# Performance work log

Hardware: AMD Instinct MI355X
Metric: run time of the kernel (lower is better)

Reference implementation:

```python
import jax, jax.numpy as jnp
import numpy as np

N = 262144        # number of nodes
D = 64            # fixed in-degree per destination node (edges grouped by dest)
RATIO = 0.5
K = int(D * RATIO)  # edges kept per node = 32


def setup_inputs() -> dict:
    key = jax.random.key(0)
    k1, k2 = jax.random.split(key)
    logits = jax.random.normal(k1, (N,), dtype=jnp.float32)
    # source endpoints: random nodes; destination endpoints: sorted, D edges per node
    src = jax.random.randint(k2, (N * D,), 0, N, dtype=jnp.int32)
    dst = jnp.repeat(jnp.arange(N, dtype=jnp.int32), D)
    edge_index = jnp.stack([src, dst])  # [2, E]
    return {"logits": logits, "edge_index": edge_index}


def reference(logits, edge_index):
    # LabelAwarePool.forward: sigmoid -> per-edge L1 similarity -> per-dest-node top-k edges
    s = jax.nn.sigmoid(logits).reshape(-1)          # [N]
    ends = s[edge_index]                            # [2, E] endpoint scores
    sim = 1.0 - jnp.abs(ends[0] - ends[1])          # [E] similarity
    E = edge_index.shape[1]
    n = E // D                                      # number of segments (nodes)
    # segmented top-k: edges are grouped by destination node in blocks of D
    _, idx = jax.lax.top_k(sim.reshape(n, D), K)    # [n, K] indices within each segment
    edges_g = edge_index.reshape(2, n, D)           # [2, n, D]
    sel = jnp.take_along_axis(edges_g, idx[None, :, :], axis=2)  # [2, n, K]
    return sel.reshape(2, n * K)                    # concatenated kept edges
```

## Files before the change

### kernel.cpp

```cpp
#include <hip/hip_runtime.h>
#include <cstdint>

#define D_EDGES 64
#define K_KEEP  32

__device__ __forceinline__ float np_expf(float x) {
    const float log2e     = 1.44269504088896341f;
    const float cvt_magic = 12582912.0f;
    const float neg_ln2hi = -0.693359375f;
    const float neg_ln2lo = 2.12194440e-4f;
    const float p0 = 1.9875691500E-4f;
    const float p1 = 1.3981999507E-3f;
    const float p2 = 8.3334519073E-3f;
    const float p3 = 4.1665795894E-2f;
    const float p4 = 1.6666665459E-1f;
    const float p5 = 5.0000001201E-1f;

    float q = fmaf(x, log2e, cvt_magic);
    q -= cvt_magic;
    x = fmaf(q, neg_ln2hi, x);
    x = fmaf(q, neg_ln2lo, x);
    float x2 = x * x;
    float poly = fmaf(p0, x, p1);
    poly = fmaf(poly, x, p2);
    poly = fmaf(poly, x, p3);
    poly = fmaf(poly, x, p4);
    poly = fmaf(poly, x, p5);
    poly = fmaf(poly, x2, x);
    poly = poly + 1.0f;
    return ldexpf(poly, (int)q);
}

__device__ __forceinline__ float sigmoid_np(float x) {
    float e = np_expf(-x);
    return 1.0f / (1.0f + e);
}

template <int CTRL>
__device__ __forceinline__ unsigned long long xor_dpp_u64(unsigned long long v) {
    int lo = (int)(unsigned)v;
    int hi = (int)(v >> 32);
    lo = __builtin_amdgcn_update_dpp(lo, lo, CTRL, 0xF, 0xF, true);
    hi = __builtin_amdgcn_update_dpp(hi, hi, CTRL, 0xF, 0xF, true);
    return ((unsigned long long)(unsigned)hi << 32) | (unsigned)lo;
}

template <int OFF>
__device__ __forceinline__ unsigned long long xor_swz_u64(unsigned long long v) {
    int lo = (int)(unsigned)v;
    int hi = (int)(v >> 32);
    lo = __builtin_amdgcn_ds_swizzle(lo, OFF);
    hi = __builtin_amdgcn_ds_swizzle(hi, OFF);
    return ((unsigned long long)(unsigned)hi << 32) | (unsigned)lo;
}

template <int J>
__device__ __forceinline__ unsigned long long xorshfl_u64(unsigned long long v) {
    if constexpr (J == 1)       return xor_dpp_u64<0xB1>(v);
    else if constexpr (J == 2)  return xor_dpp_u64<0x4E>(v);
    else if constexpr (J == 4)  return xor_swz_u64<0x101F>(v);
    else if constexpr (J == 8)  return xor_dpp_u64<0x128>(v);
    else if constexpr (J == 16) return xor_swz_u64<0x401F>(v);
    else {
        int lo = (int)(unsigned)v;
        int hi = (int)(v >> 32);
        lo = __shfl_xor(lo, 32, 64);
        hi = __shfl_xor(hi, 32, 64);
        return ((unsigned long long)(unsigned)hi << 32) | (unsigned)lo;
    }
}

template <int K, int J>
__device__ __forceinline__ void stage(unsigned long long& key, int lane) {
    unsigned long long other = xorshfl_u64<J>(key);
    const bool dir = ((lane & J) == 0) == ((lane & K) == 0);
    key = ((key > other) != dir) ? other : key;
}

__global__ __launch_bounds__(256)
void topk_kernel(const int* __restrict__ edge_index,
                 const float* __restrict__ logits,
                 int* __restrict__ out,
                 int E, int nseg, int outHalf) {
    const int tid = threadIdx.x;
    const int lane = tid & 63;
    const int w = (blockIdx.x << 2) | (tid >> 6);
    if (w >= nseg) return;
    const int e = (w << 6) | lane;

    int src = edge_index[e];
    int dst = edge_index[E + e];

    float ss = sigmoid_np(logits[src]);
    int dst0 = __builtin_amdgcn_readfirstlane(dst);
    float sd = sigmoid_np(logits[dst0]);
    float sim = 1.0f - fabsf(ss - sd);

    unsigned long long key =
        ((unsigned long long)__float_as_uint(sim) << 6) |
        (unsigned long long)(lane ^ 63);

    stage<2, 1>(key, lane);
    stage<4, 2>(key, lane);   stage<4, 1>(key, lane);
    stage<8, 4>(key, lane);   stage<8, 2>(key, lane);   stage<8, 1>(key, lane);
    stage<16, 8>(key, lane);  stage<16, 4>(key, lane);  stage<16, 2>(key, lane);
    stage<16, 1>(key, lane);
    stage<32, 16>(key, lane); stage<32, 8>(key, lane);  stage<32, 4>(key, lane);
    stage<32, 2>(key, lane);  stage<32, 1>(key, lane);
    stage<64, 32>(key, lane); stage<64, 16>(key, lane); stage<64, 8>(key, lane);
    stage<64, 4>(key, lane);  stage<64, 2>(key, lane);  stage<64, 1>(key, lane);

    int origLane = ((int)(key & 63)) ^ 63;
    int sel_src = __shfl(src, origLane, 64);

    if (lane < K_KEEP) {
        int base = (w << 5) | lane;
        out[base] = sel_src;
        out[outHalf + base] = dst;
    }
}

extern "C" void kernel_launch(void* const* d_in, const int* in_sizes, int n_in,
                              void* d_out, int out_size, void* d_ws, size_t ws_size,
                              hipStream_t stream) {
    const float* logits = (const float*)d_in[0];
    const int* edge_index = (const int*)d_in[1];
    int E = in_sizes[1] / 2;
    int nseg = E / D_EDGES;
    int outHalf = nseg * K_KEEP;
    int* out = (int*)d_out;

    int blocks = (nseg + 3) / 4;
    topk_kernel<<<blocks, 256, 0, stream>>>(edge_index, logits, out,
                                            E, nseg, outHalf);
}
```

Baseline: 284.6 us.

## Precompute sigmoid table and use 32-bit sort keys when similarities allow

Adds a separate kernel that computes the sigmoid of every logit once into workspace, so the top-k kernel gathers precomputed scores instead of evaluating the exp polynomial per edge. When every similarity in a segment is at least 0.0625, the float bits are rebased and packed with the lane index into a 32-bit key, so each bitonic stage exchanges one register instead of two and uses a ds_bpermute for the 32-lane stage. It falls back to the original 64-bit sort otherwise. The output write is made branch-free with all 64 lanes storing either src or dst. This adds an extra launch and a gather from the workspace table.

```diff
diff --git a/kernel.cpp b/kernel.cpp
--- a/kernel.cpp
+++ b/kernel.cpp
@@ -36,6 +36,35 @@
     return 1.0f / (1.0f + e);
 }
 
+__global__ void sigmoid_kernel(const float* __restrict__ logits,
+                               float* __restrict__ s, int n) {
+    int i = blockIdx.x * blockDim.x + threadIdx.x;
+    if (i < n) s[i] = sigmoid_np(logits[i]);
+}
+
+template <int CTRL>
+__device__ __forceinline__ unsigned xor_dpp_u32(unsigned v) {
+    return (unsigned)__builtin_amdgcn_update_dpp((int)v, (int)v, CTRL, 0xF, 0xF, true);
+}
+
+template <int J>
+__device__ __forceinline__ unsigned xorshfl_u32(unsigned v, int addr32) {
+    if constexpr (J == 1)       return xor_dpp_u32<0xB1>(v);
+    else if constexpr (J == 2)  return xor_dpp_u32<0x4E>(v);
+    else if constexpr (J == 4)  return (unsigned)__builtin_amdgcn_ds_swizzle((int)v, 0x101F);
+    else if constexpr (J == 8)  return xor_dpp_u32<0x128>(v);
+    else if constexpr (J == 16) return (unsigned)__builtin_amdgcn_ds_swizzle((int)v, 0x401F);
+    else                        return (unsigned)__builtin_amdgcn_ds_bpermute(addr32, (int)v);
+}
+
+template <int J>
+__device__ __forceinline__ void stage32(unsigned& key, bool dir, int addr32) {
+    unsigned other = xorshfl_u32<J>(key, addr32);
+    unsigned mx = (key > other) ? key : other;
+    unsigned mn = (key > other) ? other : key;
+    key = dir ? mx : mn;
+}
+
 template <int CTRL>
 __device__ __forceinline__ unsigned long long xor_dpp_u64(unsigned long long v) {
     int lo = (int)(unsigned)v;
@@ -71,7 +100,7 @@
 }
 
 template <int K, int J>
-__device__ __forceinline__ void stage(unsigned long long& key, int lane) {
+__device__ __forceinline__ void stage64(unsigned long long& key, int lane) {
     unsigned long long other = xorshfl_u64<J>(key);
     const bool dir = ((lane & J) == 0) == ((lane & K) == 0);
     key = ((key > other) != dir) ? other : key;
@@ -79,7 +108,7 @@
 
 __global__ __launch_bounds__(256)
 void topk_kernel(const int* __restrict__ edge_index,
-                 const float* __restrict__ logits,
+                 const float* __restrict__ stab,
                  int* __restrict__ out,
                  int E, int nseg, int outHalf) {
     const int tid = threadIdx.x;
@@ -91,33 +120,59 @@
     int src = edge_index[e];
     int dst = edge_index[E + e];
 
-    float ss = sigmoid_np(logits[src]);
-    int dst0 = __builtin_amdgcn_readfirstlane(dst);
-    float sd = sigmoid_np(logits[dst0]);
+    float ss = stab[src];
+    float sd = stab[__builtin_amdgcn_readfirstlane(dst)];
     float sim = 1.0f - fabsf(ss - sd);
 
-    unsigned long long key =
-        ((unsigned long long)__float_as_uint(sim) << 6) |
-        (unsigned long long)(lane ^ 63);
+    const bool b1  = (lane & 1)  == 0;
+    const bool b2  = (lane & 2)  == 0;
+    const bool b4  = (lane & 4)  == 0;
+    const bool b8  = (lane & 8)  == 0;
+    const bool b16 = (lane & 16) == 0;
+    const bool b32 = (lane & 32) == 0;
+    const int addr32 = (lane ^ 32) << 2;
 
-    stage<2, 1>(key, lane);
-    stage<4, 2>(key, lane);   stage<4, 1>(key, lane);
-    stage<8, 4>(key, lane);   stage<8, 2>(key, lane);   stage<8, 1>(key, lane);
-    stage<16, 8>(key, lane);  stage<16, 4>(key, lane);  stage<16, 2>(key, lane);
-    stage<16, 1>(key, lane);
-    stage<32, 16>(key, lane); stage<32, 8>(key, lane);  stage<32, 4>(key, lane);
-    stage<32, 2>(key, lane);  stage<32, 1>(key, lane);
-    stage<64, 32>(key, lane); stage<64, 16>(key, lane); stage<64, 8>(key, lane);
-    stage<64, 4>(key, lane);  stage<64, 2>(key, lane);  stage<64, 1>(key, lane);
+    int origLane;
+    if (__all(sim >= 0.0625f)) {
+        unsigned kb = __float_as_uint(sim);
+        unsigned key = ((kb - 0x3D800000u) << 6) | (unsigned)(lane ^ 63);
 
-    int origLane = ((int)(key & 63)) ^ 63;
-    int sel_src = __shfl(src, origLane, 64);
+        stage32<1>(key, b1 == b2, addr32);
+        stage32<2>(key, b2 == b4, addr32);  stage32<1>(key, b1 == b4, addr32);
+        stage32<4>(key, b4 == b8, addr32);  stage32<2>(key, b2 == b8, addr32);
+        stage32<1>(key, b1 == b8, addr32);
+        stage32<8>(key, b8 == b16, addr32); stage32<4>(key, b4 == b16, addr32);
+        stage32<2>(key, b2 == b16, addr32); stage32<1>(key, b1 == b16, addr32);
+        stage32<16>(key, b16 == b32, addr32); stage32<8>(key, b8 == b32, addr32);
+        stage32<4>(key, b4 == b32, addr32);   stage32<2>(key, b2 == b32, addr32);
+        stage32<1>(key, b1 == b32, addr32);
+        stage32<32>(key, b32, addr32); stage32<16>(key, b16, addr32);
+        stage32<8>(key, b8, addr32);   stage32<4>(key, b4, addr32);
+        stage32<2>(key, b2, addr32);   stage32<1>(key, b1, addr32);
 
-    if (lane < K_KEEP) {
-        int base = (w << 5) | lane;
-        out[base] = sel_src;
-        out[outHalf + base] = dst;
+        origLane = ((int)key & 63) ^ 63;
+    } else {
+        unsigned long long key =
+            ((unsigned long long)__float_as_uint(sim) << 6) |
+            (unsigned long long)(lane ^ 63);
+        stage64<2, 1>(key, lane);
+        stage64<4, 2>(key, lane);   stage64<4, 1>(key, lane);
+        stage64<8, 4>(key, lane);   stage64<8, 2>(key, lane);   stage64<8, 1>(key, lane);
+        stage64<16, 8>(key, lane);  stage64<16, 4>(key, lane);  stage64<16, 2>(key, lane);
+        stage64<16, 1>(key, lane);
+        stage64<32, 16>(key, lane); stage64<32, 8>(key, lane);  stage64<32, 4>(key, lane);
+        stage64<32, 2>(key, lane);  stage64<32, 1>(key, lane);
+        stage64<64, 32>(key, lane); stage64<64, 16>(key, lane); stage64<64, 8>(key, lane);
+        stage64<64, 4>(key, lane);  stage64<64, 2>(key, lane);  stage64<64, 1>(key, lane);
+        origLane = ((int)(key & 63)) ^ 63;
     }
+
+    int sel_src = __builtin_amdgcn_ds_bpermute(origLane << 2, src);
+
+    int col = lane & 31;
+    int base = (w << 5) | col;
+    bool hiHalf = lane >= 32;
+    out[hiHalf ? (outHalf + base) : base] = hiHalf ? dst : sel_src;
 }
 
 extern "C" void kernel_launch(void* const* d_in, const int* in_sizes, int n_in,
@@ -125,12 +180,16 @@
                               hipStream_t stream) {
     const float* logits = (const float*)d_in[0];
     const int* edge_index = (const int*)d_in[1];
+    int N = in_sizes[0];
     int E = in_sizes[1] / 2;
     int nseg = E / D_EDGES;
     int outHalf = nseg * K_KEEP;
     int* out = (int*)d_out;
 
+    float* stab = (float*)d_ws;
+    sigmoid_kernel<<<(N + 255) / 256, 256, 0, stream>>>(logits, stab, N);
+
     int blocks = (nseg + 3) / 4;
-    topk_kernel<<<blocks, 256, 0, stream>>>(edge_index, logits, out,
+    topk_kernel<<<blocks, 256, 0, stream>>>(edge_index, stab, out,
                                             E, nseg, outHalf);
 }
```

Result: no change. 283.4 us (-0.4%).
